# Kernel optimization log

Measured on AMD Instinct MI355X. Metric: run time of the kernel, lower is better.

The kernel has to match this reference:

```python
import jax, jax.numpy as jnp
import numpy as np
import math

PRE_NMS_TOP_N = 2000
BBOX_XFORM_CLIP = math.log(1000.0 / 16.0)
TO_REMOVE = 1.0


def _decode(rel_codes, boxes):
    widths = boxes[..., 2] - boxes[..., 0] + TO_REMOVE
    heights = boxes[..., 3] - boxes[..., 1] + TO_REMOVE
    ctr_x = boxes[..., 0] + 0.5 * widths
    ctr_y = boxes[..., 1] + 0.5 * heights

    dx = rel_codes[..., 0]
    dy = rel_codes[..., 1]
    dw = jnp.minimum(rel_codes[..., 2], BBOX_XFORM_CLIP)
    dh = jnp.minimum(rel_codes[..., 3], BBOX_XFORM_CLIP)

    pred_ctr_x = dx * widths + ctr_x
    pred_ctr_y = dy * heights + ctr_y
    pred_w = jnp.exp(dw) * widths
    pred_h = jnp.exp(dh) * heights

    x1 = pred_ctr_x - 0.5 * pred_w
    y1 = pred_ctr_y - 0.5 * pred_h
    x2 = pred_ctr_x + 0.5 * pred_w - 1.0
    y2 = pred_ctr_y + 0.5 * pred_h - 1.0
    return jnp.stack([x1, y1, x2, y2], axis=-1)


def setup_inputs() -> dict:
    key = jax.random.key(0)
    k1, k2, k3 = jax.random.split(key, 3)
    N, A = 8, 500000
    anchors = jax.random.uniform(k1, (N, A, 4), dtype=jnp.float32) * 800.0
    objectness = jax.random.normal(k2, (N, A, 1), dtype=jnp.float32)
    box_regression = jax.random.normal(k3, (N, A, 4), dtype=jnp.float32)
    return {"anchors": anchors, "objectness": objectness, "box_regression": box_regression}


def reference(anchors, objectness, box_regression):
    N, A, _ = objectness.shape
    k = min(PRE_NMS_TOP_N, A)
    scores = objectness[..., 0]                       # [N, A] (C == 1 for RPN)
    top_scores, top_idx = jax.lax.top_k(scores, k)    # sorted descending, [N, k]
    idx = top_idx[..., None]                          # [N, k, 1]
    breg = jnp.take_along_axis(box_regression, idx, axis=1)  # [N, k, 4]
    anc = jnp.take_along_axis(anchors, idx, axis=1)          # [N, k, 4]
    proposals = _decode(breg, anc)                    # [N, k, 4]
    return jnp.concatenate([proposals, top_scores[..., None]], axis=-1)  # [N, k, 5]
```

## Files before the change

### kernel.cpp

```cpp
#include <hip/hip_runtime.h>
#include <stdint.h>
#include <math.h>

#define N_BATCH 8
#define A_ELEMS 500000
#define TOPK    2000
#define NBINS   2048
#define CAP     4096
#define BCAP2   128
#define SBLK    128
#define SEG     16
#define SEGK    256
#define GRP     4
#define FBCAP   8192
#define BBOX_CLIP 4.135166556742356f


__device__ __forceinline__ uint32_t f2sortable(float f) {
    uint32_t b = __float_as_uint(f);
    return (b & 0x80000000u) ? ~b : (b | 0x80000000u);
}

__device__ __forceinline__ unsigned long long gather_key(
    const unsigned long long* pvb, const uint32_t* pre, uint32_t g) {
    int lo = 0, hi = SBLK - 1;
    while (lo < hi) { int mid = (lo + hi + 1) >> 1; if (pre[mid] <= g) lo = mid; else hi = mid - 1; }
    return pvb[(size_t)lo * BCAP2 + (g - pre[lo])];
}

__global__ __launch_bounds__(256) void scan_kernel(const float* __restrict__ obj,
                                                   uint32_t* __restrict__ bcount,
                                                   unsigned long long* __restrict__ priv) {
    __shared__ uint32_t lcount;
    const int n = blockIdx.y, blk = blockIdx.x;
    const int tid = (int)threadIdx.x;
    if (tid == 0) lcount = 0;
    __syncthreads();
    const float Tf = 2.46f;
    const float4* o4 = (const float4*)(obj + (size_t)n * A_ELEMS);
    unsigned long long* pv = priv + ((size_t)n * SBLK + blk) * BCAP2;
    const int n4 = A_ELEMS / 4;
    for (int i = blk * 256 + tid; i < n4; i += SBLK * 256) {
        float4 v = o4[i];
        float fs[4] = {v.x, v.y, v.z, v.w};
        #pragma unroll
        for (int c = 0; c < 4; ++c) {
            if (fs[c] >= Tf) {
                uint32_t pos = atomicAdd(&lcount, 1u);
                if (pos < BCAP2) {
                    uint32_t idx = (uint32_t)(i * 4 + c);
                    pv[pos] = ((unsigned long long)f2sortable(fs[c]) << 32) |
                              (unsigned long long)(~idx);
                }
            }
        }
    }
    __syncthreads();
    if (tid == 0) bcount[(size_t)n * SBLK + blk] = lcount;
}

__device__ __forceinline__ uint32_t build_prefix(
    const uint32_t* bcount, int n, int tid,
    uint32_t* cs, uint32_t* ps, uint32_t* pre, uint32_t* bad) {
    if (tid == 0) *bad = 0;
    __syncthreads();
    if (tid < SBLK) {
        uint32_t c = bcount[(size_t)n * SBLK + tid];
        cs[tid] = c; ps[tid] = c;
        if (c > BCAP2) atomicOr(bad, 1u);
    }
    __syncthreads();
    for (int off = 1; off < SBLK; off <<= 1) {
        uint32_t v = 0;
        if (tid < SBLK) { v = ps[tid]; if (tid >= off) v += ps[tid - off]; }
        __syncthreads();
        if (tid < SBLK) ps[tid] = v;
        __syncthreads();
    }
    const uint32_t total = ps[SBLK - 1];
    if (tid < SBLK) pre[tid] = ps[tid] - cs[tid];
    if (tid == 0) pre[SBLK] = total;
    __syncthreads();
    return total;
}

__global__ __launch_bounds__(256) void rank_partial_kernel(
    const uint32_t* __restrict__ bcount,
    const unsigned long long* __restrict__ priv,
    uint16_t* __restrict__ partial) {
    __shared__ unsigned long long s[SEGK];
    __shared__ uint32_t cs[SBLK], ps[SBLK], pre[SBLK + 1], bad;
    const int n = blockIdx.z, seg = blockIdx.y, grp = blockIdx.x;
    const int tid = (int)threadIdx.x;
    const uint32_t total = build_prefix(bcount, n, tid, cs, ps, pre, &bad);
    const bool okl = (bad == 0) && (total >= TOPK) && (total <= CAP);
    if (!okl) return;
    const uint32_t cnt = total;
    if ((uint32_t)(grp * 1024) >= cnt) return;
    if ((uint32_t)(seg * SEGK) >= cnt) return;
    const unsigned long long* pvb = priv + (size_t)n * SBLK * BCAP2;
    const int ks = seg * SEGK;
    for (int i = tid; i < SEGK; i += 256)
        s[i] = ((uint32_t)(ks + i) < cnt) ? gather_key(pvb, pre, ks + i) : 0ull;
    const uint32_t t0 = (uint32_t)(grp * 1024 + tid);
    const uint32_t cm = cnt - 1;
    unsigned long long k0 = gather_key(pvb, pre, t0 < cm ? t0 : cm);
    unsigned long long k1 = gather_key(pvb, pre, t0 + 256 < cm ? t0 + 256 : cm);
    unsigned long long k2 = gather_key(pvb, pre, t0 + 512 < cm ? t0 + 512 : cm);
    unsigned long long k3 = gather_key(pvb, pre, t0 + 768 < cm ? t0 + 768 : cm);
    __syncthreads();
    uint32_t r0 = 0, r1 = 0, r2 = 0, r3 = 0;
    const ulonglong2* s2 = (const ulonglong2*)s;
    #pragma unroll 8
    for (int j = 0; j < SEGK / 2; ++j) {
        ulonglong2 p = s2[j];
        r0 += (p.x > k0); r0 += (p.y > k0);
        r1 += (p.x > k1); r1 += (p.y > k1);
        r2 += (p.x > k2); r2 += (p.y > k2);
        r3 += (p.x > k3); r3 += (p.y > k3);
    }
    uint16_t* pw = partial + ((size_t)n * SEG + seg) * CAP;
    pw[t0]       = (uint16_t)r0;
    pw[t0 + 256] = (uint16_t)r1;
    pw[t0 + 512] = (uint16_t)r2;
    pw[t0 + 768] = (uint16_t)r3;
}

__global__ __launch_bounds__(256) void decode_kernel(
    const float* __restrict__ anchors, const float* __restrict__ breg,
    const float* __restrict__ obj,
    const uint32_t* __restrict__ bcount,
    unsigned long long* __restrict__ priv,
    const uint16_t* __restrict__ partial,
    float* __restrict__ out) {
    __shared__ uint32_t cs[SBLK], ps[SBLK], pre[SBLK + 1], bad;
    __shared__ uint32_t sh[NBINS];
    __shared__ uint32_t lcnt, cutb;
    const int n = blockIdx.y;
    const int tid = (int)threadIdx.x;
    const uint32_t total = build_prefix(bcount, n, tid, cs, ps, pre, &bad);
    const bool okl = (bad == 0) && (total >= TOPK) && (total <= CAP);

    if (okl) {
        const uint32_t cnt = total;
        const uint32_t t = (uint32_t)(blockIdx.x * 256 + tid);
        if (t >= cnt) return;
        const int nseg = (int)((cnt + SEGK - 1) / SEGK);
        const uint16_t* pp = partial + (size_t)n * SEG * CAP;
        uint32_t rank = 0;
        for (int sg = 0; sg < nseg; ++sg) rank += pp[(size_t)sg * CAP + t];
        if (rank >= TOPK) return;
        const unsigned long long* pvb = priv + (size_t)n * SBLK * BCAP2;
        const unsigned long long mykey = gather_key(pvb, pre, t);
        const uint32_t u    = (uint32_t)(mykey >> 32);
        const uint32_t idx  = ~((uint32_t)mykey);
        const uint32_t bits = (u & 0x80000000u) ? (u ^ 0x80000000u) : ~u;
        const float score = __uint_as_float(bits);
        const float4 a = ((const float4*)anchors)[(size_t)n * A_ELEMS + idx];
        const float4 b = ((const float4*)breg)[(size_t)n * A_ELEMS + idx];
        float w  = a.z - a.x + 1.0f;
        float h  = a.w - a.y + 1.0f;
        float cx = a.x + 0.5f * w;
        float cy = a.y + 0.5f * h;
        float dw = fminf(b.z, BBOX_CLIP);
        float dh = fminf(b.w, BBOX_CLIP);
        float pcx = b.x * w + cx;
        float pcy = b.y * h + cy;
        float pw  = expf(dw) * w;
        float ph  = expf(dh) * h;
        float* row = out + ((size_t)n * TOPK + rank) * 5;
        row[0] = pcx - 0.5f * pw;
        row[1] = pcy - 0.5f * ph;
        row[2] = pcx + 0.5f * pw - 1.0f;
        row[3] = pcy + 0.5f * ph - 1.0f;
        row[4] = score;
        return;
    }

    if (blockIdx.x != 0) return;
    for (int i = tid; i < NBINS; i += 256) sh[i] = 0;
    if (tid == 0) lcnt = 0;
    __syncthreads();
    const float* o = obj + (size_t)n * A_ELEMS;
    for (int i = tid; i < A_ELEMS; i += 256)
        atomicAdd(&sh[f2sortable(o[i]) >> 21], 1u);
    __syncthreads();
    if (tid == 0) {
        uint32_t cum = 0; int b;
        for (b = NBINS - 1; b > 0; --b) { cum += sh[b]; if (cum >= TOPK) break; }
        cutb = (uint32_t)b;
    }
    __syncthreads();
    const uint32_t cb = cutb;
    unsigned long long* fbn = priv + (size_t)n * SBLK * BCAP2;
    for (int i = tid; i < A_ELEMS; i += 256) {
        uint32_t u = f2sortable(o[i]);
        if ((u >> 21) >= cb) {
            uint32_t pos = atomicAdd(&lcnt, 1u);
            if (pos < FBCAP)
                fbn[pos] = ((unsigned long long)u << 32) | (unsigned long long)(~(uint32_t)i);
        }
    }
    __syncthreads();
    const uint32_t cnt2 = lcnt < FBCAP ? lcnt : FBCAP;
    for (uint32_t t = tid; t < cnt2; t += 256) {
        const unsigned long long myk = fbn[t];
        uint32_t rank = 0;
        for (uint32_t j = 0; j < cnt2; ++j) rank += (fbn[j] > myk);
        if (rank >= TOPK) continue;
        const uint32_t u    = (uint32_t)(myk >> 32);
        const uint32_t idx  = ~((uint32_t)myk);
        const uint32_t bits = (u & 0x80000000u) ? (u ^ 0x80000000u) : ~u;
        const float score = __uint_as_float(bits);
        const float4 a = ((const float4*)anchors)[(size_t)n * A_ELEMS + idx];
        const float4 b = ((const float4*)breg)[(size_t)n * A_ELEMS + idx];
        float w  = a.z - a.x + 1.0f;
        float h  = a.w - a.y + 1.0f;
        float cx = a.x + 0.5f * w;
        float cy = a.y + 0.5f * h;
        float dw = fminf(b.z, BBOX_CLIP);
        float dh = fminf(b.w, BBOX_CLIP);
        float pcx = b.x * w + cx;
        float pcy = b.y * h + cy;
        float pw  = expf(dw) * w;
        float ph  = expf(dh) * h;
        float* row = out + ((size_t)n * TOPK + rank) * 5;
        row[0] = pcx - 0.5f * pw;
        row[1] = pcy - 0.5f * ph;
        row[2] = pcx + 0.5f * pw - 1.0f;
        row[3] = pcy + 0.5f * ph - 1.0f;
        row[4] = score;
    }
}

extern "C" void kernel_launch(void* const* d_in, const int* in_sizes, int n_in,
                              void* d_out, int out_size, void* d_ws, size_t ws_size,
                              hipStream_t stream) {
    const float* anchors    = (const float*)d_in[0];
    const float* objectness = (const float*)d_in[1];
    const float* breg       = (const float*)d_in[2];
    float* out = (float*)d_out;

    uint8_t* ws = (uint8_t*)d_ws;
    uint32_t* bcount         = (uint32_t*)ws;
    unsigned long long* priv = (unsigned long long*)(ws + 4096);
    uint16_t* partial        = (uint16_t*)(ws + 1052672);

    dim3 g1(SBLK, N_BATCH);
    scan_kernel<<<g1, 256, 0, stream>>>(objectness, bcount, priv);
    dim3 g2(GRP, SEG, N_BATCH);
    rank_partial_kernel<<<g2, 256, 0, stream>>>(bcount, priv, partial);
    dim3 g3(CAP / 256, N_BATCH);
    decode_kernel<<<g3, 256, 0, stream>>>(anchors, breg, objectness, bcount, priv,
                                          partial, out);
}
```

Baseline: 149.5 us.

## Replace all-pairs rank kernels with in-block bucket sort and decode

The separate partial-rank kernel and the decode kernel become one 1024-thread block per batch. That block buckets the candidate keys by their high score bits into a shared-memory histogram, computes bucket offsets with a prefix scan, scatters the keys, and ranks each key only against its own bucket before decoding. This removes a kernel launch and the O(n^2) pairwise comparisons over about 4K candidates. In exchange, only 8 blocks do the work, and a bucket holding many equal high bits would bring quadratic cost back within that bucket.

```diff
diff --git a/kernel.cpp b/kernel.cpp
--- a/kernel.cpp
+++ b/kernel.cpp
@@ -9,10 +9,9 @@
 #define CAP     4096
 #define BCAP2   128
 #define SBLK    128
-#define SEG     16
-#define SEGK    256
-#define GRP     4
 #define FBCAP   8192
+#define NB2     2048
+#define SHIFT2  13
 #define BBOX_CLIP 4.135166556742356f
 
 
@@ -26,6 +25,33 @@
     int lo = 0, hi = SBLK - 1;
     while (lo < hi) { int mid = (lo + hi + 1) >> 1; if (pre[mid] <= g) lo = mid; else hi = mid - 1; }
     return pvb[(size_t)lo * BCAP2 + (g - pre[lo])];
+}
+
+__device__ __forceinline__ void decode_write(
+    const float* anchors, const float* breg, int n,
+    unsigned long long key, uint32_t rank, float* out) {
+    const uint32_t u    = (uint32_t)(key >> 32);
+    const uint32_t idx  = ~((uint32_t)key);
+    const uint32_t bits = (u & 0x80000000u) ? (u ^ 0x80000000u) : ~u;
+    const float score = __uint_as_float(bits);
+    const float4 a = ((const float4*)anchors)[(size_t)n * A_ELEMS + idx];
+    const float4 b = ((const float4*)breg)[(size_t)n * A_ELEMS + idx];
+    float w  = a.z - a.x + 1.0f;
+    float h  = a.w - a.y + 1.0f;
+    float cx = a.x + 0.5f * w;
+    float cy = a.y + 0.5f * h;
+    float dw = fminf(b.z, BBOX_CLIP);
+    float dh = fminf(b.w, BBOX_CLIP);
+    float pcx = b.x * w + cx;
+    float pcy = b.y * h + cy;
+    float pw  = expf(dw) * w;
+    float ph  = expf(dh) * h;
+    float* row = out + ((size_t)n * TOPK + rank) * 5;
+    row[0] = pcx - 0.5f * pw;
+    row[1] = pcy - 0.5f * ph;
+    row[2] = pcx + 0.5f * pw - 1.0f;
+    row[3] = pcy + 0.5f * ph - 1.0f;
+    row[4] = score;
 }
 
 __global__ __launch_bounds__(256) void scan_kernel(const float* __restrict__ obj,
@@ -59,141 +85,124 @@
     if (tid == 0) bcount[(size_t)n * SBLK + blk] = lcount;
 }
 
-__device__ __forceinline__ uint32_t build_prefix(
-    const uint32_t* bcount, int n, int tid,
-    uint32_t* cs, uint32_t* ps, uint32_t* pre, uint32_t* bad) {
-    if (tid == 0) *bad = 0;
-    __syncthreads();
-    if (tid < SBLK) {
-        uint32_t c = bcount[(size_t)n * SBLK + tid];
-        cs[tid] = c; ps[tid] = c;
-        if (c > BCAP2) atomicOr(bad, 1u);
-    }
-    __syncthreads();
-    for (int off = 1; off < SBLK; off <<= 1) {
-        uint32_t v = 0;
-        if (tid < SBLK) { v = ps[tid]; if (tid >= off) v += ps[tid - off]; }
-        __syncthreads();
-        if (tid < SBLK) ps[tid] = v;
-        __syncthreads();
-    }
-    const uint32_t total = ps[SBLK - 1];
-    if (tid < SBLK) pre[tid] = ps[tid] - cs[tid];
-    if (tid == 0) pre[SBLK] = total;
-    __syncthreads();
-    return total;
-}
-
-__global__ __launch_bounds__(256) void rank_partial_kernel(
-    const uint32_t* __restrict__ bcount,
-    const unsigned long long* __restrict__ priv,
-    uint16_t* __restrict__ partial) {
-    __shared__ unsigned long long s[SEGK];
-    __shared__ uint32_t cs[SBLK], ps[SBLK], pre[SBLK + 1], bad;
-    const int n = blockIdx.z, seg = blockIdx.y, grp = blockIdx.x;
-    const int tid = (int)threadIdx.x;
-    const uint32_t total = build_prefix(bcount, n, tid, cs, ps, pre, &bad);
-    const bool okl = (bad == 0) && (total >= TOPK) && (total <= CAP);
-    if (!okl) return;
-    const uint32_t cnt = total;
-    if ((uint32_t)(grp * 1024) >= cnt) return;
-    if ((uint32_t)(seg * SEGK) >= cnt) return;
-    const unsigned long long* pvb = priv + (size_t)n * SBLK * BCAP2;
-    const int ks = seg * SEGK;
-    for (int i = tid; i < SEGK; i += 256)
-        s[i] = ((uint32_t)(ks + i) < cnt) ? gather_key(pvb, pre, ks + i) : 0ull;
-    const uint32_t t0 = (uint32_t)(grp * 1024 + tid);
-    const uint32_t cm = cnt - 1;
-    unsigned long long k0 = gather_key(pvb, pre, t0 < cm ? t0 : cm);
-    unsigned long long k1 = gather_key(pvb, pre, t0 + 256 < cm ? t0 + 256 : cm);
-    unsigned long long k2 = gather_key(pvb, pre, t0 + 512 < cm ? t0 + 512 : cm);
-    unsigned long long k3 = gather_key(pvb, pre, t0 + 768 < cm ? t0 + 768 : cm);
-    __syncthreads();
-    uint32_t r0 = 0, r1 = 0, r2 = 0, r3 = 0;
-    const ulonglong2* s2 = (const ulonglong2*)s;
-    #pragma unroll 8
-    for (int j = 0; j < SEGK / 2; ++j) {
-        ulonglong2 p = s2[j];
-        r0 += (p.x > k0); r0 += (p.y > k0);
-        r1 += (p.x > k1); r1 += (p.y > k1);
-        r2 += (p.x > k2); r2 += (p.y > k2);
-        r3 += (p.x > k3); r3 += (p.y > k3);
-    }
-    uint16_t* pw = partial + ((size_t)n * SEG + seg) * CAP;
-    pw[t0]       = (uint16_t)r0;
-    pw[t0 + 256] = (uint16_t)r1;
-    pw[t0 + 512] = (uint16_t)r2;
-    pw[t0 + 768] = (uint16_t)r3;
-}
-
-__global__ __launch_bounds__(256) void decode_kernel(
+__global__ __launch_bounds__(1024) void sortdecode_kernel(
     const float* __restrict__ anchors, const float* __restrict__ breg,
     const float* __restrict__ obj,
     const uint32_t* __restrict__ bcount,
     unsigned long long* __restrict__ priv,
-    const uint16_t* __restrict__ partial,
     float* __restrict__ out) {
-    __shared__ uint32_t cs[SBLK], ps[SBLK], pre[SBLK + 1], bad;
-    __shared__ uint32_t sh[NBINS];
+    __shared__ uint32_t cs[SBLK], ps[SBLK], pre[SBLK + 1];
+    __shared__ uint32_t bad;
+    __shared__ uint32_t hist[NB2];
+    __shared__ uint32_t boff[NB2];
+    __shared__ uint32_t bcur[NB2];
+    __shared__ uint32_t ws2[1024];
+    __shared__ unsigned long long s[CAP];
     __shared__ uint32_t lcnt, cutb;
-    const int n = blockIdx.y;
+    const int n = blockIdx.x;
     const int tid = (int)threadIdx.x;
-    const uint32_t total = build_prefix(bcount, n, tid, cs, ps, pre, &bad);
-    const bool okl = (bad == 0) && (total >= TOPK) && (total <= CAP);
+
+    if (tid == 0) bad = 0;
+    __syncthreads();
+    if (tid < SBLK) {
+        uint32_t c = bcount[(size_t)n * SBLK + tid];
+        cs[tid] = c; ps[tid] = c;
+        if (c > BCAP2) atomicOr(&bad, 1u);
+    }
+    __syncthreads();
+    for (int off = 1; off < SBLK; off <<= 1) {
+        uint32_t v = 0;
+        if (tid < SBLK) { v = ps[tid]; if (tid >= off) v += ps[tid - off]; }
+        __syncthreads();
+        if (tid < SBLK) ps[tid] = v;
+        __syncthreads();
+    }
+    const uint32_t total = (tid < SBLK) ? 0u : 0u;
+    __syncthreads();
+    const uint32_t cnt_all = ps[SBLK - 1];
+    if (tid < SBLK) pre[tid] = ps[tid] - cs[tid];
+    if (tid == 0) pre[SBLK] = cnt_all;
+    __syncthreads();
+    const bool okl = (bad == 0) && (cnt_all >= TOPK) && (cnt_all <= CAP);
 
     if (okl) {
-        const uint32_t cnt = total;
-        const uint32_t t = (uint32_t)(blockIdx.x * 256 + tid);
-        if (t >= cnt) return;
-        const int nseg = (int)((cnt + SEGK - 1) / SEGK);
-        const uint16_t* pp = partial + (size_t)n * SEG * CAP;
-        uint32_t rank = 0;
-        for (int sg = 0; sg < nseg; ++sg) rank += pp[(size_t)sg * CAP + t];
-        if (rank >= TOPK) return;
+        const uint32_t cnt = cnt_all;
+        for (int i = tid; i < NB2; i += 1024) hist[i] = 0;
+        __syncthreads();
         const unsigned long long* pvb = priv + (size_t)n * SBLK * BCAP2;
-        const unsigned long long mykey = gather_key(pvb, pre, t);
-        const uint32_t u    = (uint32_t)(mykey >> 32);
-        const uint32_t idx  = ~((uint32_t)mykey);
-        const uint32_t bits = (u & 0x80000000u) ? (u ^ 0x80000000u) : ~u;
-        const float score = __uint_as_float(bits);
-        const float4 a = ((const float4*)anchors)[(size_t)n * A_ELEMS + idx];
-        const float4 b = ((const float4*)breg)[(size_t)n * A_ELEMS + idx];
-        float w  = a.z - a.x + 1.0f;
-        float h  = a.w - a.y + 1.0f;
-        float cx = a.x + 0.5f * w;
-        float cy = a.y + 0.5f * h;
-        float dw = fminf(b.z, BBOX_CLIP);
-        float dh = fminf(b.w, BBOX_CLIP);
-        float pcx = b.x * w + cx;
-        float pcy = b.y * h + cy;
-        float pw  = expf(dw) * w;
-        float ph  = expf(dh) * h;
-        float* row = out + ((size_t)n * TOPK + rank) * 5;
-        row[0] = pcx - 0.5f * pw;
-        row[1] = pcy - 0.5f * ph;
-        row[2] = pcx + 0.5f * pw - 1.0f;
-        row[3] = pcy + 0.5f * ph - 1.0f;
-        row[4] = score;
+        const uint32_t BASE = f2sortable(2.46f) >> SHIFT2;
+        unsigned long long kk[4];
+        uint32_t kb[4];
+        #pragma unroll
+        for (int i = 0; i < 4; ++i) {
+            const uint32_t g = (uint32_t)tid + (uint32_t)i * 1024u;
+            kb[i] = 0xFFFFFFFFu;
+            if (g < cnt) {
+                unsigned long long k = gather_key(pvb, pre, g);
+                uint32_t d = ((uint32_t)(k >> 32) >> SHIFT2) - BASE;
+                if (d > (NB2 - 1)) d = NB2 - 1;
+                const uint32_t rbin = (NB2 - 1) - d;
+                kk[i] = k; kb[i] = rbin;
+                atomicAdd(&hist[rbin], 1u);
+            }
+        }
+        __syncthreads();
+        const uint32_t h0 = hist[2 * tid], h1 = hist[2 * tid + 1];
+        const uint32_t sum2 = h0 + h1;
+        ws2[tid] = sum2;
+        __syncthreads();
+        for (int off = 1; off < 1024; off <<= 1) {
+            uint32_t v = ws2[tid];
+            uint32_t w = (tid >= off) ? ws2[tid - off] : 0u;
+            __syncthreads();
+            ws2[tid] = v + w;
+            __syncthreads();
+        }
+        const uint32_t base2 = ws2[tid] - sum2;
+        boff[2 * tid]     = base2;
+        bcur[2 * tid]     = base2;
+        boff[2 * tid + 1] = base2 + h0;
+        bcur[2 * tid + 1] = base2 + h0;
+        __syncthreads();
+        #pragma unroll
+        for (int i = 0; i < 4; ++i) {
+            if (kb[i] != 0xFFFFFFFFu) {
+                uint32_t slot = atomicAdd(&bcur[kb[i]], 1u);
+                s[slot] = kk[i];
+            }
+        }
+        __syncthreads();
+        #pragma unroll
+        for (int i = 0; i < 4; ++i) {
+            if (kb[i] == 0xFFFFFFFFu) continue;
+            const uint32_t lo = boff[kb[i]];
+            const uint32_t sz = hist[kb[i]];
+            const unsigned long long mk = kk[i];
+            uint32_t r = 0;
+            for (uint32_t j = lo; j < lo + sz; ++j) r += (s[j] > mk);
+            const uint32_t pos = lo + r;
+            if (pos < TOPK)
+                decode_write(anchors, breg, n, mk, pos, out);
+        }
         return;
     }
 
-    if (blockIdx.x != 0) return;
-    for (int i = tid; i < NBINS; i += 256) sh[i] = 0;
+    for (int i = tid; i < NBINS; i += 1024) hist[i] = 0;
     if (tid == 0) lcnt = 0;
     __syncthreads();
     const float* o = obj + (size_t)n * A_ELEMS;
-    for (int i = tid; i < A_ELEMS; i += 256)
-        atomicAdd(&sh[f2sortable(o[i]) >> 21], 1u);
+    for (int i = tid; i < A_ELEMS; i += 1024)
+        atomicAdd(&hist[f2sortable(o[i]) >> 21], 1u);
     __syncthreads();
     if (tid == 0) {
         uint32_t cum = 0; int b;
-        for (b = NBINS - 1; b > 0; --b) { cum += sh[b]; if (cum >= TOPK) break; }
+        for (b = NBINS - 1; b > 0; --b) { cum += hist[b]; if (cum >= TOPK) break; }
         cutb = (uint32_t)b;
     }
     __syncthreads();
     const uint32_t cb = cutb;
     unsigned long long* fbn = priv + (size_t)n * SBLK * BCAP2;
-    for (int i = tid; i < A_ELEMS; i += 256) {
+    for (int i = tid; i < A_ELEMS; i += 1024) {
         uint32_t u = f2sortable(o[i]);
         if ((u >> 21) >= cb) {
             uint32_t pos = atomicAdd(&lcnt, 1u);
@@ -203,33 +212,12 @@
     }
     __syncthreads();
     const uint32_t cnt2 = lcnt < FBCAP ? lcnt : FBCAP;
-    for (uint32_t t = tid; t < cnt2; t += 256) {
+    for (uint32_t t = tid; t < cnt2; t += 1024) {
         const unsigned long long myk = fbn[t];
         uint32_t rank = 0;
         for (uint32_t j = 0; j < cnt2; ++j) rank += (fbn[j] > myk);
-        if (rank >= TOPK) continue;
-        const uint32_t u    = (uint32_t)(myk >> 32);
-        const uint32_t idx  = ~((uint32_t)myk);
-        const uint32_t bits = (u & 0x80000000u) ? (u ^ 0x80000000u) : ~u;
-        const float score = __uint_as_float(bits);
-        const float4 a = ((const float4*)anchors)[(size_t)n * A_ELEMS + idx];
-        const float4 b = ((const float4*)breg)[(size_t)n * A_ELEMS + idx];
-        float w  = a.z - a.x + 1.0f;
-        float h  = a.w - a.y + 1.0f;
-        float cx = a.x + 0.5f * w;
-        float cy = a.y + 0.5f * h;
-        float dw = fminf(b.z, BBOX_CLIP);
-        float dh = fminf(b.w, BBOX_CLIP);
-        float pcx = b.x * w + cx;
-        float pcy = b.y * h + cy;
-        float pw  = expf(dw) * w;
-        float ph  = expf(dh) * h;
-        float* row = out + ((size_t)n * TOPK + rank) * 5;
-        row[0] = pcx - 0.5f * pw;
-        row[1] = pcy - 0.5f * ph;
-        row[2] = pcx + 0.5f * pw - 1.0f;
-        row[3] = pcy + 0.5f * ph - 1.0f;
-        row[4] = score;
+        if (rank < TOPK)
+            decode_write(anchors, breg, n, myk, rank, out);
     }
 }
 
@@ -244,13 +232,9 @@
     uint8_t* ws = (uint8_t*)d_ws;
     uint32_t* bcount         = (uint32_t*)ws;
     unsigned long long* priv = (unsigned long long*)(ws + 4096);
-    uint16_t* partial        = (uint16_t*)(ws + 1052672);
 
     dim3 g1(SBLK, N_BATCH);
     scan_kernel<<<g1, 256, 0, stream>>>(objectness, bcount, priv);
-    dim3 g2(GRP, SEG, N_BATCH);
-    rank_partial_kernel<<<g2, 256, 0, stream>>>(bcount, priv, partial);
-    dim3 g3(CAP / 256, N_BATCH);
-    decode_kernel<<<g3, 256, 0, stream>>>(anchors, breg, objectness, bcount, priv,
-                                          partial, out);
-}
+    sortdecode_kernel<<<N_BATCH, 1024, 0, stream>>>(anchors, breg, objectness,
+                                                    bcount, priv, out);
+}
```

New measurement: 153.6 us. 1.03x slower.
